# Kernel optimization log

Measured on AMD Instinct MI355X. Metric: run time of the kernel, lower is better.

## Reference

```python
import jax, jax.numpy as jnp
import numpy as np

N = 50000
E = 800000
IN_DIM, HID, OUT = 128, 256, 256


def setup_inputs() -> dict:
    key = jax.random.key(0)
    ks = jax.random.split(key, 6)
    x = jax.random.normal(ks[0], (N, IN_DIM), dtype=jnp.float32)
    edge_index = jax.random.randint(ks[1], (2, E), 0, N, dtype=jnp.int64)
    W1 = jax.random.normal(ks[2], (IN_DIM, HID), dtype=jnp.float32) / np.sqrt(IN_DIM)
    b1 = jnp.zeros((HID,), dtype=jnp.float32)
    W2 = jax.random.normal(ks[3], (HID, OUT), dtype=jnp.float32) / np.sqrt(HID)
    b2 = jnp.zeros((OUT,), dtype=jnp.float32)
    return {"x": x, "edge_index": edge_index, "W1": W1, "b1": b1, "W2": W2, "b2": b2}


def _gcn_conv(x, edge_index, W, b):
    """PyG GCNConv: add self-loops, symmetric deg^-1/2 norm, linear, scatter-add, bias."""
    n = x.shape[0]
    loops = jnp.arange(n, dtype=edge_index.dtype)
    src = jnp.concatenate([edge_index[0], loops])  # [E+N]
    dst = jnp.concatenate([edge_index[1], loops])  # [E+N]
    deg = jax.ops.segment_sum(jnp.ones(src.shape[0], dtype=x.dtype), dst, num_segments=n)
    dinv = jnp.where(deg > 0, jax.lax.rsqrt(deg), jnp.zeros_like(deg))
    norm = dinv[src] * dinv[dst]  # [E+N]
    h = x @ W  # [N, out] small GEMM before gather (PyG order)
    msg = h[src] * norm[:, None]  # [E+N, out] -- dominant memory traffic
    out = jax.ops.segment_sum(msg, dst, num_segments=n)
    return out + b


def reference(x, edge_index, W1, b1, W2, b2):
    h = jax.nn.relu(_gcn_conv(x, edge_index, W1, b1))
    # dropout is identity in eval mode
    out = _gcn_conv(h, edge_index, W2, b2)
    # F.normalize(p=2, dim=-1, eps=1e-12)
    nrm = jnp.maximum(jnp.linalg.norm(out, axis=-1, keepdims=True), 1e-12)
    return out / nrm
```

## Files before the change

kernel.cpp:

```cpp
#include <hip/hip_runtime.h>
#include <hip/hip_bf16.h>


#define NNODE 50000
#define FDIM 256
#define SCAN_CHUNK 2048

typedef __attribute__((ext_vector_type(8))) short short8;
typedef __attribute__((ext_vector_type(4))) float f32x4;

__device__ __forceinline__ float bf2f(unsigned short u) {
    union { unsigned int i; float f; } c;
    c.i = ((unsigned int)u) << 16;
    return c.f;
}
__device__ __forceinline__ float bflo(unsigned int u) {
    union { unsigned int i; float f; } c;
    c.i = u << 16;
    return c.f;
}
__device__ __forceinline__ float bfhi(unsigned int u) {
    union { unsigned int i; float f; } c;
    c.i = u & 0xFFFF0000u;
    return c.f;
}
__device__ __forceinline__ unsigned short f2bf(float f) {
    __hip_bfloat16 h = __float2bfloat16(f);
    return *reinterpret_cast<unsigned short*>(&h);
}

__global__ void count_kernel(const int* __restrict__ ei, int* __restrict__ counts, int E) {
    int e = blockIdx.x * blockDim.x + threadIdx.x;
    if (e < E) atomicAdd(&counts[ei[E + e]], 1);
}

__global__ __launch_bounds__(256) void scan_part1(const int* __restrict__ counts,
                                                  int* __restrict__ bsum, int n) {
    __shared__ int ws[4];
    int b = blockIdx.x, t = threadIdx.x;
    int base = b * SCAN_CHUNK + t * 8;
    int s = 0;
#pragma unroll
    for (int j = 0; j < 8; ++j) {
        int i = base + j;
        if (i < n) s += counts[i];
    }
#pragma unroll
    for (int off = 32; off >= 1; off >>= 1) s += __shfl_xor(s, off, 64);
    if ((t & 63) == 0) ws[t >> 6] = s;
    __syncthreads();
    if (t == 0) bsum[b] = ws[0] + ws[1] + ws[2] + ws[3];
}

__global__ void scan_part2(const int* __restrict__ bsum, int* __restrict__ boff,
                           int* __restrict__ row_ptr, int nb, int n) {
    int l = threadIdx.x;
    int v = (l < nb) ? bsum[l] : 0;
    int incl = v;
#pragma unroll
    for (int off = 1; off < 64; off <<= 1) {
        int u = __shfl_up(incl, off, 64);
        if (l >= off) incl += u;
    }
    if (l < nb) boff[l] = incl - v;
    if (l == nb - 1) row_ptr[n] = incl;
}

__global__ __launch_bounds__(256) void scan_part3(const int* __restrict__ counts,
                                                  const int* __restrict__ boff,
                                                  int* __restrict__ row_ptr,
                                                  int* __restrict__ cursor,
                                                  float* __restrict__ dinv, int n) {
    __shared__ int ws[4];
    int b = blockIdx.x, t = threadIdx.x, lane = t & 63, wid = t >> 6;
    int base = b * SCAN_CHUNK + t * 8;
    int v[8];
    int s = 0;
#pragma unroll
    for (int j = 0; j < 8; ++j) {
        int i = base + j;
        v[j] = (i < n) ? counts[i] : 0;
        s += v[j];
    }
    int incl = s;
#pragma unroll
    for (int off = 1; off < 64; off <<= 1) {
        int u = __shfl_up(incl, off, 64);
        if (lane >= off) incl += u;
    }
    if (lane == 63) ws[wid] = incl;
    __syncthreads();
    int woff = 0;
    for (int u = 0; u < wid; ++u) woff += ws[u];
    int ex = boff[b] + woff + incl - s;
#pragma unroll
    for (int j = 0; j < 8; ++j) {
        int i = base + j;
        if (i < n) {
            row_ptr[i] = ex;
            cursor[i] = ex;
            dinv[i] = rsqrtf((float)(v[j] + 1));
        }
        ex += v[j];
    }
}

__global__ void fill_kernel(const int* __restrict__ ei, const float* __restrict__ dinv,
                            int* __restrict__ cursor, int2* __restrict__ edata, int E) {
    int e = blockIdx.x * blockDim.x + threadIdx.x;
    if (e < E) {
        int s = ei[e];
        int d = ei[E + e];
        int pos = atomicAdd(&cursor[d], 1);
        float nm = dinv[s] * dinv[d];
        edata[pos] = make_int2(s, __float_as_int(nm));
    }
}

__global__ void wconv_kernel(const float* __restrict__ W1, unsigned short* __restrict__ Wf1,
                             const float* __restrict__ W2, unsigned short* __restrict__ Wf2) {
    int idx = blockIdx.x * blockDim.x + threadIdx.x;
    const float* W;
    unsigned short* Wf;
    if (idx < 16 * 256) {
        W = W1; Wf = Wf1;
    } else if (idx < (16 + 32) * 256) {
        idx -= 16 * 256;
        W = W2; Wf = Wf2;
    } else {
        return;
    }
    int g = idx >> 8, c = idx & 255;
    ushort4 lo = make_ushort4(f2bf(W[(8 * g + 0) * 256 + c]), f2bf(W[(8 * g + 1) * 256 + c]),
                              f2bf(W[(8 * g + 2) * 256 + c]), f2bf(W[(8 * g + 3) * 256 + c]));
    ushort4 hi = make_ushort4(f2bf(W[(8 * g + 4) * 256 + c]), f2bf(W[(8 * g + 5) * 256 + c]),
                              f2bf(W[(8 * g + 6) * 256 + c]), f2bf(W[(8 * g + 7) * 256 + c]));
    *reinterpret_cast<ushort4*>(&Wf[(size_t)idx * 8]) = lo;
    *reinterpret_cast<ushort4*>(&Wf[(size_t)idx * 8 + 4]) = hi;
}

template <int K, typename T>
__global__ __launch_bounds__(256) void gemm_mfma(const T* __restrict__ X,
                                                 const unsigned short* __restrict__ Wf,
                                                 unsigned short* __restrict__ H, int n) {
    __shared__ unsigned short As[64 * K];
    int t = threadIdx.x;
    int row0 = blockIdx.x * 64;

    if constexpr (sizeof(T) == 4) {
#pragma unroll
        for (int i = 0; i < (64 * K) / (4 * 256); ++i) {
            int o = 4 * (t + 256 * i);
            int row = o / K, k = o % K;
            int srow = row0 + row;
            float4 v = make_float4(0.f, 0.f, 0.f, 0.f);
            if (srow < n) v = *reinterpret_cast<const float4*>(&X[(size_t)srow * K + k]);
            ushort4 p = make_ushort4(f2bf(v.x), f2bf(v.y), f2bf(v.z), f2bf(v.w));
            int gx = (k >> 3) ^ (row & 7);
            *reinterpret_cast<ushort4*>(&As[row * K + gx * 8 + (k & 7)]) = p;
        }
    } else {
#pragma unroll
        for (int i = 0; i < (64 * K) / (8 * 256); ++i) {
            int o = 8 * (t + 256 * i);
            int row = o / K, k = o % K;
            int srow = row0 + row;
            uint4 v = make_uint4(0u, 0u, 0u, 0u);
            if (srow < n) v = *reinterpret_cast<const uint4*>(&X[(size_t)srow * K + k]);
            int gx = (k >> 3) ^ (row & 7);
            *reinterpret_cast<uint4*>(&As[row * K + gx * 8]) = v;
        }
    }
    __syncthreads();

    int lane = t & 63, wv = t >> 6;
    int l15 = lane & 15, lhi = lane >> 4;
    f32x4 zero = {0.f, 0.f, 0.f, 0.f};
    f32x4 acc[4][4];
#pragma unroll
    for (int rf = 0; rf < 4; ++rf)
#pragma unroll
        for (int cf = 0; cf < 4; ++cf) acc[rf][cf] = zero;

#pragma unroll
    for (int s = 0; s < K / 32; ++s) {
        int g = 4 * s + lhi;
        short8 a[4], b[4];
#pragma unroll
        for (int rf = 0; rf < 4; ++rf) {
            int row = 16 * rf + l15;
            a[rf] = *reinterpret_cast<const short8*>(&As[row * K + (g ^ (row & 7)) * 8]);
        }
#pragma unroll
        for (int cf = 0; cf < 4; ++cf) {
            int c = 64 * wv + 16 * cf + l15;
            b[cf] = *reinterpret_cast<const short8*>(&Wf[((size_t)g * 256 + c) * 8]);
        }
#pragma unroll
        for (int rf = 0; rf < 4; ++rf)
#pragma unroll
            for (int cf = 0; cf < 4; ++cf)
                acc[rf][cf] = __builtin_amdgcn_mfma_f32_16x16x32_bf16(a[rf], b[cf], acc[rf][cf], 0, 0, 0);
    }

#pragma unroll
    for (int rf = 0; rf < 4; ++rf)
#pragma unroll
        for (int cf = 0; cf < 4; ++cf) {
            f32x4 a = acc[rf][cf];
            int col = 64 * wv + 16 * cf + l15;
#pragma unroll
            for (int j = 0; j < 4; ++j) {
                int row = row0 + 16 * rf + 4 * lhi + j;
                if (row < n) H[(size_t)row * 256 + col] = f2bf(a[j]);
            }
        }
}

__device__ __forceinline__ void agg_core(const unsigned short* __restrict__ hb,
                                         const int* __restrict__ rowp,
                                         const int2* __restrict__ edata,
                                         const float* __restrict__ dinv,
                                         const float* __restrict__ bias,
                                         int node, int lane, float acc[8]) {
    int half = lane >> 5;
    int l31 = lane & 31;
    float di = dinv[node];
    float scale = half ? 0.f : 1.f;
    float d2 = di * di * scale;
    uint4 sv = *(reinterpret_cast<const uint4*>(hb + (size_t)node * FDIM) + l31);
    float4 bv0 = *(reinterpret_cast<const float4*>(bias) + 2 * l31);
    float4 bv1 = *(reinterpret_cast<const float4*>(bias) + 2 * l31 + 1);
    acc[0] = fmaf(bflo(sv.x), d2, bv0.x * scale);
    acc[1] = fmaf(bfhi(sv.x), d2, bv0.y * scale);
    acc[2] = fmaf(bflo(sv.y), d2, bv0.z * scale);
    acc[3] = fmaf(bfhi(sv.y), d2, bv0.w * scale);
    acc[4] = fmaf(bflo(sv.z), d2, bv1.x * scale);
    acc[5] = fmaf(bfhi(sv.z), d2, bv1.y * scale);
    acc[6] = fmaf(bflo(sv.w), d2, bv1.z * scale);
    acc[7] = fmaf(bfhi(sv.w), d2, bv1.w * scale);
    int beg = rowp[node], end = rowp[node + 1];
#pragma unroll 2
    for (int e = beg; e < end; e += 2) {
        int ee = e + half;
        bool valid = ee < end;
        int2 ed = edata[valid ? ee : e];
        float nm = valid ? __int_as_float(ed.y) : 0.f;
        int src = valid ? ed.x : node;
        uint4 v = *(reinterpret_cast<const uint4*>(hb + (size_t)src * FDIM) + l31);
        acc[0] = fmaf(bflo(v.x), nm, acc[0]);
        acc[1] = fmaf(bfhi(v.x), nm, acc[1]);
        acc[2] = fmaf(bflo(v.y), nm, acc[2]);
        acc[3] = fmaf(bfhi(v.y), nm, acc[3]);
        acc[4] = fmaf(bflo(v.z), nm, acc[4]);
        acc[5] = fmaf(bfhi(v.z), nm, acc[5]);
        acc[6] = fmaf(bflo(v.w), nm, acc[6]);
        acc[7] = fmaf(bfhi(v.w), nm, acc[7]);
    }
#pragma unroll
    for (int j = 0; j < 8; ++j) acc[j] += __shfl_xor(acc[j], 32, 64);
}

__global__ __launch_bounds__(256) void agg_relu_kernel(const unsigned short* __restrict__ hb,
                                                       const int* __restrict__ rowp,
                                                       const int2* __restrict__ edata,
                                                       const float* __restrict__ dinv,
                                                       const float* __restrict__ bias,
                                                       unsigned short* __restrict__ outB, int n) {
    int node = (blockIdx.x * blockDim.x + threadIdx.x) >> 6;
    int lane = threadIdx.x & 63;
    if (node >= n) return;
    float acc[8];
    agg_core(hb, rowp, edata, dinv, bias, node, lane, acc);
    int half = lane >> 5, l31 = lane & 63 & 31;
    int j0 = 4 * half;
    ushort4 o = make_ushort4(f2bf(fmaxf(acc[j0 + 0], 0.f)), f2bf(fmaxf(acc[j0 + 1], 0.f)),
                             f2bf(fmaxf(acc[j0 + 2], 0.f)), f2bf(fmaxf(acc[j0 + 3], 0.f)));
    *reinterpret_cast<ushort4*>(outB + (size_t)node * FDIM + l31 * 8 + j0) = o;
}

__global__ __launch_bounds__(256) void agg_norm_kernel(const unsigned short* __restrict__ hb,
                                                       const int* __restrict__ rowp,
                                                       const int2* __restrict__ edata,
                                                       const float* __restrict__ dinv,
                                                       const float* __restrict__ bias,
                                                       float* __restrict__ out, int n) {
    int node = (blockIdx.x * blockDim.x + threadIdx.x) >> 6;
    int lane = threadIdx.x & 63;
    if (node >= n) return;
    float acc[8];
    agg_core(hb, rowp, edata, dinv, bias, node, lane, acc);
    float ss = 0.f;
#pragma unroll
    for (int j = 0; j < 8; ++j) ss = fmaf(acc[j], acc[j], ss);
#pragma unroll
    for (int off = 16; off >= 1; off >>= 1) ss += __shfl_xor(ss, off, 64);
    float rinv = 1.f / fmaxf(sqrtf(ss), 1e-12f);
    int half = lane >> 5, l31 = lane & 31;
    int j0 = 4 * half;
    f32x4 o = {acc[j0 + 0] * rinv, acc[j0 + 1] * rinv, acc[j0 + 2] * rinv, acc[j0 + 3] * rinv};
    __builtin_nontemporal_store(o, reinterpret_cast<f32x4*>(out + (size_t)node * FDIM + l31 * 8 + j0));
}

extern "C" void kernel_launch(void* const* d_in, const int* in_sizes, int n_in,
                              void* d_out, int out_size, void* d_ws, size_t ws_size,
                              hipStream_t stream) {
    const float* x  = (const float*)d_in[0];
    const int*   ei = (const int*)d_in[1];
    const float* W1 = (const float*)d_in[2];
    const float* b1 = (const float*)d_in[3];
    const float* W2 = (const float*)d_in[4];
    const float* b2 = (const float*)d_in[5];
    float* out = (float*)d_out;

    const int N = NNODE;
    const int E = in_sizes[1] / 2;
    const int NB = (N + SCAN_CHUNK - 1) / SCAN_CHUNK;

    char* ws = (char*)d_ws;
    size_t off = 0;
    auto alloc = [&](size_t bytes) -> void* {
        void* p = ws + off;
        off = (off + bytes + 255) & ~(size_t)255;
        return p;
    };
    unsigned short* Hbf = (unsigned short*)alloc((size_t)N * FDIM * 2);
    unsigned short* Bbf = (unsigned short*)alloc((size_t)N * FDIM * 2);
    unsigned short* Wf1 = (unsigned short*)alloc((size_t)(128 / 8) * 256 * 8 * 2);
    unsigned short* Wf2 = (unsigned short*)alloc((size_t)(256 / 8) * 256 * 8 * 2);
    int*   counts = (int*)alloc((size_t)N * 4);
    int*   rowp   = (int*)alloc((size_t)(N + 1) * 4);
    int*   cursor = (int*)alloc((size_t)N * 4);
    float* dinv   = (float*)alloc((size_t)N * 4);
    int2*  edata  = (int2*)alloc((size_t)E * 8);
    int*   bsum   = (int*)alloc((size_t)NB * 4);
    int*   boff   = (int*)alloc((size_t)NB * 4);

    wconv_kernel<<<(48 * 256 + 255) / 256, 256, 0, stream>>>(W1, Wf1, W2, Wf2);

    hipMemsetAsync(counts, 0, (size_t)N * 4, stream);
    count_kernel<<<(E + 255) / 256, 256, 0, stream>>>(ei, counts, E);
    scan_part1<<<NB, 256, 0, stream>>>(counts, bsum, N);
    scan_part2<<<1, 64, 0, stream>>>(bsum, boff, rowp, NB, N);
    scan_part3<<<NB, 256, 0, stream>>>(counts, boff, rowp, cursor, dinv, N);
    fill_kernel<<<(E + 255) / 256, 256, 0, stream>>>(ei, dinv, cursor, edata, E);

    gemm_mfma<128, float><<<(N + 63) / 64, 256, 0, stream>>>(x, Wf1, Hbf, N);
    agg_relu_kernel<<<(N * 64 + 255) / 256, 256, 0, stream>>>(Hbf, rowp, edata, dinv, b1, Bbf, N);
    gemm_mfma<256, unsigned short><<<(N + 63) / 64, 256, 0, stream>>>(Bbf, Wf2, Hbf, N);
    agg_norm_kernel<<<(N * 64 + 255) / 256, 256, 0, stream>>>(Hbf, rowp, edata, dinv, b2, out, N);
}
```

Measured before the change: 253.1 us.

## Aggregate before GEMM and fuse bias/ReLU/normalize into GEMM epilogues

Reorders each GCN layer to aggregate first and then multiply by W (A·X·W = A·(X)·W), so layer 1 gathers 128-wide bf16 rows of x instead of 256-wide H rows. Bias+ReLU and bias+L2-normalize move into the GEMM epilogues, with a shared-memory cross-wave row-norm reduction. x casting, weight conversion and degree counting are merged into one prep kernel. Rounding order changes slightly because aggregation now happens on bf16 inputs rather than on bf16 products.

```diff
diff --git a/kernel.cpp b/kernel.cpp
--- a/kernel.cpp
+++ b/kernel.cpp
@@ -5,15 +5,12 @@
 #define NNODE 50000
 #define FDIM 256
 #define SCAN_CHUNK 2048
+#define CAST_BLOCKS 3125
+#define WCONV_BLOCKS 48
 
 typedef __attribute__((ext_vector_type(8))) short short8;
 typedef __attribute__((ext_vector_type(4))) float f32x4;
 
-__device__ __forceinline__ float bf2f(unsigned short u) {
-    union { unsigned int i; float f; } c;
-    c.i = ((unsigned int)u) << 16;
-    return c.f;
-}
 __device__ __forceinline__ float bflo(unsigned int u) {
     union { unsigned int i; float f; } c;
     c.i = u << 16;
@@ -28,10 +25,41 @@
     __hip_bfloat16 h = __float2bfloat16(f);
     return *reinterpret_cast<unsigned short*>(&h);
 }
-
-__global__ void count_kernel(const int* __restrict__ ei, int* __restrict__ counts, int E) {
-    int e = blockIdx.x * blockDim.x + threadIdx.x;
-    if (e < E) atomicAdd(&counts[ei[E + e]], 1);
+__device__ __forceinline__ unsigned int pk(float lo, float hi) {
+    return (unsigned int)f2bf(lo) | ((unsigned int)f2bf(hi) << 16);
+}
+
+__global__ __launch_bounds__(256) void prep_kernel(
+    const float* __restrict__ x, unsigned int* __restrict__ xb,
+    const float* __restrict__ W1, unsigned short* __restrict__ Wf1,
+    const float* __restrict__ W2, unsigned short* __restrict__ Wf2,
+    const int* __restrict__ ei, int* __restrict__ counts, int E) {
+    int b = blockIdx.x, t = threadIdx.x;
+    if (b < CAST_BLOCKS) {
+        int i = b * 256 + t;
+        const float4* xf = reinterpret_cast<const float4*>(x);
+        float4 p = xf[2 * i], q = xf[2 * i + 1];
+        uint4 o;
+        o.x = pk(p.x, p.y); o.y = pk(p.z, p.w);
+        o.z = pk(q.x, q.y); o.w = pk(q.z, q.w);
+        reinterpret_cast<uint4*>(xb)[i] = o;
+    } else if (b < CAST_BLOCKS + WCONV_BLOCKS) {
+        int idx = (b - CAST_BLOCKS) * 256 + t;
+        const float* W;
+        unsigned short* Wf;
+        if (idx < 16 * 256) { W = W1; Wf = Wf1; }
+        else { idx -= 16 * 256; W = W2; Wf = Wf2; }
+        int g = idx >> 8, c = idx & 255;
+        ushort4 lo = make_ushort4(f2bf(W[(8 * g + 0) * 256 + c]), f2bf(W[(8 * g + 1) * 256 + c]),
+                                  f2bf(W[(8 * g + 2) * 256 + c]), f2bf(W[(8 * g + 3) * 256 + c]));
+        ushort4 hi = make_ushort4(f2bf(W[(8 * g + 4) * 256 + c]), f2bf(W[(8 * g + 5) * 256 + c]),
+                                  f2bf(W[(8 * g + 6) * 256 + c]), f2bf(W[(8 * g + 7) * 256 + c]));
+        *reinterpret_cast<ushort4*>(&Wf[(size_t)idx * 8]) = lo;
+        *reinterpret_cast<ushort4*>(&Wf[(size_t)idx * 8 + 4]) = hi;
+    } else {
+        int e = (b - CAST_BLOCKS - WCONV_BLOCKS) * 256 + t;
+        if (e < E) atomicAdd(&counts[ei[E + e]], 1);
+    }
 }
 
 __global__ __launch_bounds__(256) void scan_part1(const int* __restrict__ counts,
@@ -117,59 +145,97 @@
     }
 }
 
-__global__ void wconv_kernel(const float* __restrict__ W1, unsigned short* __restrict__ Wf1,
-                             const float* __restrict__ W2, unsigned short* __restrict__ Wf2) {
-    int idx = blockIdx.x * blockDim.x + threadIdx.x;
-    const float* W;
-    unsigned short* Wf;
-    if (idx < 16 * 256) {
-        W = W1; Wf = Wf1;
-    } else if (idx < (16 + 32) * 256) {
-        idx -= 16 * 256;
-        W = W2; Wf = Wf2;
-    } else {
-        return;
-    }
-    int g = idx >> 8, c = idx & 255;
-    ushort4 lo = make_ushort4(f2bf(W[(8 * g + 0) * 256 + c]), f2bf(W[(8 * g + 1) * 256 + c]),
-                              f2bf(W[(8 * g + 2) * 256 + c]), f2bf(W[(8 * g + 3) * 256 + c]));
-    ushort4 hi = make_ushort4(f2bf(W[(8 * g + 4) * 256 + c]), f2bf(W[(8 * g + 5) * 256 + c]),
-                              f2bf(W[(8 * g + 6) * 256 + c]), f2bf(W[(8 * g + 7) * 256 + c]));
-    *reinterpret_cast<ushort4*>(&Wf[(size_t)idx * 8]) = lo;
-    *reinterpret_cast<ushort4*>(&Wf[(size_t)idx * 8 + 4]) = hi;
-}
-
-template <int K, typename T>
-__global__ __launch_bounds__(256) void gemm_mfma(const T* __restrict__ X,
-                                                 const unsigned short* __restrict__ Wf,
-                                                 unsigned short* __restrict__ H, int n) {
+__global__ __launch_bounds__(256) void agg1_kernel(const unsigned int* __restrict__ xb,
+                                                   const int* __restrict__ rowp,
+                                                   const int2* __restrict__ edata,
+                                                   const float* __restrict__ dinv,
+                                                   unsigned int* __restrict__ A1, int n) {
+    int node = (blockIdx.x << 2) + (threadIdx.x >> 6);
+    if (node >= n) return;
+    int lane = threadIdx.x & 63;
+    float di = dinv[node];
+    float d2 = di * di;
+    unsigned int sv = xb[(size_t)node * 64 + lane];
+    float a0 = bflo(sv) * d2, a1 = bfhi(sv) * d2;
+    int beg = rowp[node], end = rowp[node + 1];
+    for (int e = beg; e < end; e += 4) {
+        int2 ed[4];
+        unsigned int v[4];
+#pragma unroll
+        for (int k = 0; k < 4; ++k) {
+            int ee = e + k;
+            ed[k] = (ee < end) ? edata[ee] : make_int2(node, 0);
+        }
+#pragma unroll
+        for (int k = 0; k < 4; ++k) v[k] = xb[(size_t)ed[k].x * 64 + lane];
+#pragma unroll
+        for (int k = 0; k < 4; ++k) {
+            float nm = __int_as_float(ed[k].y);
+            a0 = fmaf(bflo(v[k]), nm, a0);
+            a1 = fmaf(bfhi(v[k]), nm, a1);
+        }
+    }
+    A1[(size_t)node * 64 + lane] = pk(a0, a1);
+}
+
+__global__ __launch_bounds__(256) void agg2_kernel(const uint2* __restrict__ hb,
+                                                   const int* __restrict__ rowp,
+                                                   const int2* __restrict__ edata,
+                                                   const float* __restrict__ dinv,
+                                                   uint2* __restrict__ A2, int n) {
+    int node = (blockIdx.x << 2) + (threadIdx.x >> 6);
+    if (node >= n) return;
+    int lane = threadIdx.x & 63;
+    float di = dinv[node];
+    float d2 = di * di;
+    uint2 sv = hb[(size_t)node * 64 + lane];
+    float a0 = bflo(sv.x) * d2, a1 = bfhi(sv.x) * d2;
+    float a2 = bflo(sv.y) * d2, a3 = bfhi(sv.y) * d2;
+    int beg = rowp[node], end = rowp[node + 1];
+    for (int e = beg; e < end; e += 4) {
+        int2 ed[4];
+        uint2 v[4];
+#pragma unroll
+        for (int k = 0; k < 4; ++k) {
+            int ee = e + k;
+            ed[k] = (ee < end) ? edata[ee] : make_int2(node, 0);
+        }
+#pragma unroll
+        for (int k = 0; k < 4; ++k) v[k] = hb[(size_t)ed[k].x * 64 + lane];
+#pragma unroll
+        for (int k = 0; k < 4; ++k) {
+            float nm = __int_as_float(ed[k].y);
+            a0 = fmaf(bflo(v[k].x), nm, a0);
+            a1 = fmaf(bfhi(v[k].x), nm, a1);
+            a2 = fmaf(bflo(v[k].y), nm, a2);
+            a3 = fmaf(bfhi(v[k].y), nm, a3);
+        }
+    }
+    uint2 o;
+    o.x = pk(a0, a1);
+    o.y = pk(a2, a3);
+    A2[(size_t)node * 64 + lane] = o;
+}
+
+template <int K, int EPI>
+__global__ __launch_bounds__(256) void gemm_fused(const unsigned short* __restrict__ A,
+                                                  const unsigned short* __restrict__ Wf,
+                                                  const float* __restrict__ bias,
+                                                  void* __restrict__ outp, int n) {
     __shared__ unsigned short As[64 * K];
+    __shared__ __align__(16) float ssred[64][4];
     int t = threadIdx.x;
     int row0 = blockIdx.x * 64;
 
-    if constexpr (sizeof(T) == 4) {
-#pragma unroll
-        for (int i = 0; i < (64 * K) / (4 * 256); ++i) {
-            int o = 4 * (t + 256 * i);
-            int row = o / K, k = o % K;
-            int srow = row0 + row;
-            float4 v = make_float4(0.f, 0.f, 0.f, 0.f);
-            if (srow < n) v = *reinterpret_cast<const float4*>(&X[(size_t)srow * K + k]);
-            ushort4 p = make_ushort4(f2bf(v.x), f2bf(v.y), f2bf(v.z), f2bf(v.w));
-            int gx = (k >> 3) ^ (row & 7);
-            *reinterpret_cast<ushort4*>(&As[row * K + gx * 8 + (k & 7)]) = p;
-        }
-    } else {
-#pragma unroll
-        for (int i = 0; i < (64 * K) / (8 * 256); ++i) {
-            int o = 8 * (t + 256 * i);
-            int row = o / K, k = o % K;
-            int srow = row0 + row;
-            uint4 v = make_uint4(0u, 0u, 0u, 0u);
-            if (srow < n) v = *reinterpret_cast<const uint4*>(&X[(size_t)srow * K + k]);
-            int gx = (k >> 3) ^ (row & 7);
-            *reinterpret_cast<uint4*>(&As[row * K + gx * 8]) = v;
-        }
+#pragma unroll
+    for (int i = 0; i < (64 * K) / (8 * 256); ++i) {
+        int o = 8 * (t + 256 * i);
+        int row = o / K, k = o % K;
+        int srow = row0 + row;
+        uint4 v = make_uint4(0u, 0u, 0u, 0u);
+        if (srow < n) v = *reinterpret_cast<const uint4*>(&A[(size_t)srow * K + k]);
+        int gx = (k >> 3) ^ (row & 7);
+        *reinterpret_cast<uint4*>(&As[row * K + gx * 8]) = v;
     }
     __syncthreads();
 
@@ -203,103 +269,77 @@
                 acc[rf][cf] = __builtin_amdgcn_mfma_f32_16x16x32_bf16(a[rf], b[cf], acc[rf][cf], 0, 0, 0);
     }
 
-#pragma unroll
-    for (int rf = 0; rf < 4; ++rf)
+    if constexpr (EPI == 0) {
+        unsigned short* H = (unsigned short*)outp;
 #pragma unroll
         for (int cf = 0; cf < 4; ++cf) {
-            f32x4 a = acc[rf][cf];
             int col = 64 * wv + 16 * cf + l15;
+            float bc = bias[col];
+#pragma unroll
+            for (int rf = 0; rf < 4; ++rf) {
+#pragma unroll
+                for (int j = 0; j < 4; ++j) {
+                    int row = row0 + 16 * rf + 4 * lhi + j;
+                    if (row < n) H[(size_t)row * 256 + col] = f2bf(fmaxf(acc[rf][cf][j] + bc, 0.f));
+                }
+            }
+        }
+    } else {
+        float* O = (float*)outp;
+        float ss[4][4];
+#pragma unroll
+        for (int rf = 0; rf < 4; ++rf)
+#pragma unroll
+            for (int j = 0; j < 4; ++j) ss[rf][j] = 0.f;
+#pragma unroll
+        for (int cf = 0; cf < 4; ++cf) {
+            int col = 64 * wv + 16 * cf + l15;
+            float bc = bias[col];
+#pragma unroll
+            for (int rf = 0; rf < 4; ++rf)
+#pragma unroll
+                for (int j = 0; j < 4; ++j) {
+                    float v = acc[rf][cf][j] + bc;
+                    acc[rf][cf][j] = v;
+                    ss[rf][j] = fmaf(v, v, ss[rf][j]);
+                }
+        }
+#pragma unroll
+        for (int rf = 0; rf < 4; ++rf)
 #pragma unroll
             for (int j = 0; j < 4; ++j) {
-                int row = row0 + 16 * rf + 4 * lhi + j;
-                if (row < n) H[(size_t)row * 256 + col] = f2bf(a[j]);
+#pragma unroll
+                for (int off = 1; off <= 8; off <<= 1)
+                    ss[rf][j] += __shfl_xor(ss[rf][j], off, 64);
             }
-        }
-}
-
-__device__ __forceinline__ void agg_core(const unsigned short* __restrict__ hb,
-                                         const int* __restrict__ rowp,
-                                         const int2* __restrict__ edata,
-                                         const float* __restrict__ dinv,
-                                         const float* __restrict__ bias,
-                                         int node, int lane, float acc[8]) {
-    int half = lane >> 5;
-    int l31 = lane & 31;
-    float di = dinv[node];
-    float scale = half ? 0.f : 1.f;
-    float d2 = di * di * scale;
-    uint4 sv = *(reinterpret_cast<const uint4*>(hb + (size_t)node * FDIM) + l31);
-    float4 bv0 = *(reinterpret_cast<const float4*>(bias) + 2 * l31);
-    float4 bv1 = *(reinterpret_cast<const float4*>(bias) + 2 * l31 + 1);
-    acc[0] = fmaf(bflo(sv.x), d2, bv0.x * scale);
-    acc[1] = fmaf(bfhi(sv.x), d2, bv0.y * scale);
-    acc[2] = fmaf(bflo(sv.y), d2, bv0.z * scale);
-    acc[3] = fmaf(bfhi(sv.y), d2, bv0.w * scale);
-    acc[4] = fmaf(bflo(sv.z), d2, bv1.x * scale);
-    acc[5] = fmaf(bfhi(sv.z), d2, bv1.y * scale);
-    acc[6] = fmaf(bflo(sv.w), d2, bv1.z * scale);
-    acc[7] = fmaf(bfhi(sv.w), d2, bv1.w * scale);
-    int beg = rowp[node], end = rowp[node + 1];
-#pragma unroll 2
-    for (int e = beg; e < end; e += 2) {
-        int ee = e + half;
-        bool valid = ee < end;
-        int2 ed = edata[valid ? ee : e];
-        float nm = valid ? __int_as_float(ed.y) : 0.f;
-        int src = valid ? ed.x : node;
-        uint4 v = *(reinterpret_cast<const uint4*>(hb + (size_t)src * FDIM) + l31);
-        acc[0] = fmaf(bflo(v.x), nm, acc[0]);
-        acc[1] = fmaf(bfhi(v.x), nm, acc[1]);
-        acc[2] = fmaf(bflo(v.y), nm, acc[2]);
-        acc[3] = fmaf(bfhi(v.y), nm, acc[3]);
-        acc[4] = fmaf(bflo(v.z), nm, acc[4]);
-        acc[5] = fmaf(bfhi(v.z), nm, acc[5]);
-        acc[6] = fmaf(bflo(v.w), nm, acc[6]);
-        acc[7] = fmaf(bfhi(v.w), nm, acc[7]);
-    }
-#pragma unroll
-    for (int j = 0; j < 8; ++j) acc[j] += __shfl_xor(acc[j], 32, 64);
-}
-
-__global__ __launch_bounds__(256) void agg_relu_kernel(const unsigned short* __restrict__ hb,
-                                                       const int* __restrict__ rowp,
-                                                       const int2* __restrict__ edata,
-                                                       const float* __restrict__ dinv,
-                                                       const float* __restrict__ bias,
-                                                       unsigned short* __restrict__ outB, int n) {
-    int node = (blockIdx.x * blockDim.x + threadIdx.x) >> 6;
-    int lane = threadIdx.x & 63;
-    if (node >= n) return;
-    float acc[8];
-    agg_core(hb, rowp, edata, dinv, bias, node, lane, acc);
-    int half = lane >> 5, l31 = lane & 63 & 31;
-    int j0 = 4 * half;
-    ushort4 o = make_ushort4(f2bf(fmaxf(acc[j0 + 0], 0.f)), f2bf(fmaxf(acc[j0 + 1], 0.f)),
-                             f2bf(fmaxf(acc[j0 + 2], 0.f)), f2bf(fmaxf(acc[j0 + 3], 0.f)));
-    *reinterpret_cast<ushort4*>(outB + (size_t)node * FDIM + l31 * 8 + j0) = o;
-}
-
-__global__ __launch_bounds__(256) void agg_norm_kernel(const unsigned short* __restrict__ hb,
-                                                       const int* __restrict__ rowp,
-                                                       const int2* __restrict__ edata,
-                                                       const float* __restrict__ dinv,
-                                                       const float* __restrict__ bias,
-                                                       float* __restrict__ out, int n) {
-    int node = (blockIdx.x * blockDim.x + threadIdx.x) >> 6;
-    int lane = threadIdx.x & 63;
-    if (node >= n) return;
-    float acc[8];
-    agg_core(hb, rowp, edata, dinv, bias, node, lane, acc);
-    float ss = 0.f;
-#pragma unroll
-    for (int j = 0; j < 8; ++j) ss = fmaf(acc[j], acc[j], ss);
-#pragma unroll
-    for (int off = 16; off >= 1; off >>= 1) ss += __shfl_xor(ss, off, 64);
-    float rinv = 1.f / fmaxf(sqrtf(ss), 1e-12f);
-    int half = lane >> 5, l31 = lane & 31;
-    int j0 = 4 * half;
-    f32x4 o = {acc[j0 + 0] * rinv, acc[j0 + 1] * rinv, acc[j0 + 2] * rinv, acc[j0 + 3] * rinv};
-    __builtin_nontemporal_store(o, reinterpret_cast<f32x4*>(out + (size_t)node * FDIM + l31 * 8 + j0));
+        if (l15 == 0) {
+#pragma unroll
+            for (int rf = 0; rf < 4; ++rf)
+#pragma unroll
+                for (int j = 0; j < 4; ++j) ssred[16 * rf + 4 * lhi + j][wv] = ss[rf][j];
+        }
+        __syncthreads();
+        float rinv[4][4];
+#pragma unroll
+        for (int rf = 0; rf < 4; ++rf)
+#pragma unroll
+            for (int j = 0; j < 4; ++j) {
+                float4 s4 = *reinterpret_cast<const float4*>(ssred[16 * rf + 4 * lhi + j]);
+                float tot = s4.x + s4.y + s4.z + s4.w;
+                rinv[rf][j] = 1.f / fmaxf(sqrtf(tot), 1e-12f);
+            }
+#pragma unroll
+        for (int cf = 0; cf < 4; ++cf) {
+            int col = 64 * wv + 16 * cf + l15;
+#pragma unroll
+            for (int rf = 0; rf < 4; ++rf)
+#pragma unroll
+                for (int j = 0; j < 4; ++j) {
+                    int row = row0 + 16 * rf + 4 * lhi + j;
+                    if (row < n) O[(size_t)row * 256 + col] = acc[rf][cf][j] * rinv[rf][j];
+                }
+        }
+    }
 }
 
 extern "C" void kernel_launch(void* const* d_in, const int* in_sizes, int n_in,
@@ -324,10 +364,12 @@
         off = (off + bytes + 255) & ~(size_t)255;
         return p;
     };
-    unsigned short* Hbf = (unsigned short*)alloc((size_t)N * FDIM * 2);
+    unsigned int*   xb  = (unsigned int*)alloc((size_t)N * 128 * 2);
+    unsigned int*   A1  = (unsigned int*)alloc((size_t)N * 128 * 2);
     unsigned short* Bbf = (unsigned short*)alloc((size_t)N * FDIM * 2);
-    unsigned short* Wf1 = (unsigned short*)alloc((size_t)(128 / 8) * 256 * 8 * 2);
-    unsigned short* Wf2 = (unsigned short*)alloc((size_t)(256 / 8) * 256 * 8 * 2);
+    uint2*          A2  = (uint2*)alloc((size_t)N * FDIM * 2);
+    unsigned short* Wf1 = (unsigned short*)alloc((size_t)16 * 256 * 8 * 2);
+    unsigned short* Wf2 = (unsigned short*)alloc((size_t)32 * 256 * 8 * 2);
     int*   counts = (int*)alloc((size_t)N * 4);
     int*   rowp   = (int*)alloc((size_t)(N + 1) * 4);
     int*   cursor = (int*)alloc((size_t)N * 4);
@@ -336,17 +378,20 @@
     int*   bsum   = (int*)alloc((size_t)NB * 4);
     int*   boff   = (int*)alloc((size_t)NB * 4);
 
-    wconv_kernel<<<(48 * 256 + 255) / 256, 256, 0, stream>>>(W1, Wf1, W2, Wf2);
-
     hipMemsetAsync(counts, 0, (size_t)N * 4, stream);
-    count_kernel<<<(E + 255) / 256, 256, 0, stream>>>(ei, counts, E);
+    int count_blocks = (E + 255) / 256;
+    prep_kernel<<<CAST_BLOCKS + WCONV_BLOCKS + count_blocks, 256, 0, stream>>>(
+        x, xb, W1, Wf1, W2, Wf2, ei, counts, E);
     scan_part1<<<NB, 256, 0, stream>>>(counts, bsum, N);
     scan_part2<<<1, 64, 0, stream>>>(bsum, boff, rowp, NB, N);
     scan_part3<<<NB, 256, 0, stream>>>(counts, boff, rowp, cursor, dinv, N);
     fill_kernel<<<(E + 255) / 256, 256, 0, stream>>>(ei, dinv, cursor, edata, E);
 
-    gemm_mfma<128, float><<<(N + 63) / 64, 256, 0, stream>>>(x, Wf1, Hbf, N);
-    agg_relu_kernel<<<(N * 64 + 255) / 256, 256, 0, stream>>>(Hbf, rowp, edata, dinv, b1, Bbf, N);
-    gemm_mfma<256, unsigned short><<<(N + 63) / 64, 256, 0, stream>>>(Bbf, Wf2, Hbf, N);
-    agg_norm_kernel<<<(N * 64 + 255) / 256, 256, 0, stream>>>(Hbf, rowp, edata, dinv, b2, out, N);
-}
+    agg1_kernel<<<(N + 3) / 4, 256, 0, stream>>>(xb, rowp, edata, dinv, A1, N);
+    gemm_fused<128, 0><<<(N + 63) / 64, 256, 0, stream>>>(
+        (const unsigned short*)A1, Wf1, b1, Bbf, N);
+    agg2_kernel<<<(N + 3) / 4, 256, 0, stream>>>(
+        (const uint2*)Bbf, rowp, edata, dinv, A2, N);
+    gemm_fused<256, 1><<<(N + 63) / 64, 256, 0, stream>>>(
+        (const unsigned short*)A2, Wf2, b2, out, N);
+}
```

Result: slower. 281.0 us (+11.1%).
